# Kernel tuning notes

Hardware: AMD Instinct MI355X
Metric: run time of the kernel (lower is better)

## Reference

```python
import jax, jax.numpy as jnp
from jax import lax
import numpy as np

T, B, I, H, L, O = 512, 64, 256, 512, 2, 256


def _lstm_layer(x_seq, h0, c0, W_ih, W_hh, b_ih, b_hh):
    # x_seq: [T,B,in], W_ih: [4H,in], W_hh: [4H,H]
    pre = jnp.einsum('tbi,gi->tbg', x_seq, W_ih) + b_ih  # [T,B,4H]

    def step(carry, p):
        h, c = carry
        g = p + h @ W_hh.T + b_hh          # [B,4H], PyTorch gate order i,f,g,o
        i, f, gg, o = jnp.split(g, 4, axis=-1)
        i = jax.nn.sigmoid(i)
        f = jax.nn.sigmoid(f)
        gg = jnp.tanh(gg)
        o = jax.nn.sigmoid(o)
        c = f * c + i * gg
        h = o * jnp.tanh(c)
        return (h, c), h

    _, hs = lax.scan(step, (h0, c0), pre)
    return hs  # [T,B,H]


def setup_inputs() -> dict:
    key = jax.random.key(0)
    ks = jax.random.split(key, 12)
    s = 1.0 / np.sqrt(H)
    u = lambda k, shape: jax.random.uniform(k, shape, jnp.float32, -s, s)
    inp = {
        'input': jax.random.normal(ks[0], (T, B, I), jnp.float32),
        'hidden_cell': jnp.zeros((2, L, B, H), jnp.float32),
        'W_ih0': u(ks[1], (4 * H, I)),
        'W_hh0': u(ks[2], (4 * H, H)),
        'b_ih0': u(ks[3], (4 * H,)),
        'b_hh0': u(ks[4], (4 * H,)),
        'W_ih1': u(ks[5], (4 * H, H)),
        'W_hh1': u(ks[6], (4 * H, H)),
        'b_ih1': u(ks[7], (4 * H,)),
        'b_hh1': u(ks[8], (4 * H,)),
        'W_out': u(ks[9], (O, H)),
        'b_out': u(ks[10], (O,)),
    }
    return inp


def reference(input, hidden_cell, W_ih0, W_hh0, b_ih0, b_hh0,
              W_ih1, W_hh1, b_ih1, b_hh1, W_out, b_out):
    h0, c0 = hidden_cell[0], hidden_cell[1]  # each [L,B,H]
    hs0 = _lstm_layer(input, h0[0], c0[0], W_ih0, W_hh0, b_ih0, b_hh0)
    hs1 = _lstm_layer(hs0, h0[1], c0[1], W_ih1, W_hh1, b_ih1, b_hh1)
    # c2o applied to output at final timestep
    return hs1[-1] @ W_out.T + b_out  # [B,O]
```

## Files before the change

kernel.cpp:

```cpp
#include <hip/hip_runtime.h>

typedef _Float16 half8 __attribute__((ext_vector_type(8)));
typedef _Float16 half4 __attribute__((ext_vector_type(4)));
typedef float floatx4 __attribute__((ext_vector_type(4)));
typedef unsigned uintx4 __attribute__((ext_vector_type(4)));
typedef unsigned long long u64;

#define T_STEPS 512
#define IN_DIM 256
#define HID 512
#define RING 8


__device__ inline float sig_f(float x) { return 1.f / (1.f + __expf(-x)); }
__device__ inline float tanh_f(float x) {
  float t = __expf(-2.f * fabsf(x));
  return copysignf((1.f - t) / (1.f + t), x);
}
__device__ inline unsigned umin_(unsigned a, unsigned b) { return a < b ? a : b; }

__device__ inline void cstore_pair(_Float16* p, float a, float b) {
  union { unsigned u; _Float16 h[2]; } pk;
  pk.h[0] = (_Float16)a; pk.h[1] = (_Float16)b;
  __hip_atomic_store((unsigned*)p, pk.u, __ATOMIC_RELAXED, __HIP_MEMORY_SCOPE_AGENT);
}
__device__ inline void cstore64(_Float16* p, u64 v) {
  __hip_atomic_store((u64*)p, v, __ATOMIC_RELAXED, __HIP_MEMORY_SCOPE_AGENT);
}
__device__ inline u64 cload64(const _Float16* p) {
  return __hip_atomic_load((const u64*)p, __ATOMIC_RELAXED, __HIP_MEMORY_SCOPE_AGENT);
}
__device__ inline half8 cload_h8(const _Float16* p) {
  union { u64 u[2]; half8 v; } r;
  r.u[0] = cload64(p);
  r.u[1] = cload64(p + 4);
  return r.v;
}

__device__ inline void ldfrag16(const char* b0, half8 (&r)[16]) {
  const char* b1 = b0 + 4096;
  const char* b2 = b0 + 8192;
  const char* b3 = b0 + 12288;
  floatx4 t0, t1, t2, t3, t4, t5, t6, t7, t8, t9, t10, t11, t12, t13, t14, t15;
  asm volatile(
      "global_load_dwordx4 %0, %16, off sc0 sc1\n\t"
      "global_load_dwordx4 %1, %16, off offset:1024 sc0 sc1\n\t"
      "global_load_dwordx4 %2, %16, off offset:2048 sc0 sc1\n\t"
      "global_load_dwordx4 %3, %16, off offset:3072 sc0 sc1\n\t"
      "global_load_dwordx4 %4, %17, off sc0 sc1\n\t"
      "global_load_dwordx4 %5, %17, off offset:1024 sc0 sc1\n\t"
      "global_load_dwordx4 %6, %17, off offset:2048 sc0 sc1\n\t"
      "global_load_dwordx4 %7, %17, off offset:3072 sc0 sc1\n\t"
      "global_load_dwordx4 %8, %18, off sc0 sc1\n\t"
      "global_load_dwordx4 %9, %18, off offset:1024 sc0 sc1\n\t"
      "global_load_dwordx4 %10, %18, off offset:2048 sc0 sc1\n\t"
      "global_load_dwordx4 %11, %18, off offset:3072 sc0 sc1\n\t"
      "global_load_dwordx4 %12, %19, off sc0 sc1\n\t"
      "global_load_dwordx4 %13, %19, off offset:1024 sc0 sc1\n\t"
      "global_load_dwordx4 %14, %19, off offset:2048 sc0 sc1\n\t"
      "global_load_dwordx4 %15, %19, off offset:3072 sc0 sc1\n\t"
      "s_waitcnt vmcnt(0)"
      : "=&v"(t0), "=&v"(t1), "=&v"(t2), "=&v"(t3),
        "=&v"(t4), "=&v"(t5), "=&v"(t6), "=&v"(t7),
        "=&v"(t8), "=&v"(t9), "=&v"(t10), "=&v"(t11),
        "=&v"(t12), "=&v"(t13), "=&v"(t14), "=&v"(t15)
      : "v"(b0), "v"(b1), "v"(b2), "v"(b3)
      : "memory");
  r[0] = __builtin_bit_cast(half8, t0);   r[1] = __builtin_bit_cast(half8, t1);
  r[2] = __builtin_bit_cast(half8, t2);   r[3] = __builtin_bit_cast(half8, t3);
  r[4] = __builtin_bit_cast(half8, t4);   r[5] = __builtin_bit_cast(half8, t5);
  r[6] = __builtin_bit_cast(half8, t6);   r[7] = __builtin_bit_cast(half8, t7);
  r[8] = __builtin_bit_cast(half8, t8);   r[9] = __builtin_bit_cast(half8, t9);
  r[10] = __builtin_bit_cast(half8, t10); r[11] = __builtin_bit_cast(half8, t11);
  r[12] = __builtin_bit_cast(half8, t12); r[13] = __builtin_bit_cast(half8, t13);
  r[14] = __builtin_bit_cast(half8, t14); r[15] = __builtin_bit_cast(half8, t15);
}

__device__ inline void waitf4(const unsigned* fg, unsigned tg) {
  if (tg == 0) return;
  const unsigned* p = fg + (threadIdx.x & 63) * 32;
  int it = 0;
  for (;;) {
    floatx4 t;
    asm volatile("global_load_dwordx4 %0, %1, off sc0 sc1\n\t"
                 "s_waitcnt vmcnt(0)"
                 : "=&v"(t) : "v"(p) : "memory");
    uintx4 u = __builtin_bit_cast(uintx4, t);
    unsigned m = umin_(umin_(u.x, u.y), umin_(u.z, u.w));
    if (__all((int)(m >= tg))) return;
    if (++it > 4) __builtin_amdgcn_s_sleep(1);
  }
}

__device__ inline bool waitf4_dual(const unsigned* fg1, unsigned tg1,
                                   const unsigned* fg0, unsigned tg0) {
  const unsigned* p1 = fg1 + (threadIdx.x & 63) * 32;
  const unsigned* p0 = fg0 + (threadIdx.x & 63) * 32;
  unsigned m1, m0v;
  int it = 0;
  for (;;) {
    floatx4 t1, t0;
    asm volatile("global_load_dwordx4 %0, %2, off sc0 sc1\n\t"
                 "global_load_dwordx4 %1, %3, off sc0 sc1\n\t"
                 "s_waitcnt vmcnt(0)"
                 : "=&v"(t1), "=&v"(t0)
                 : "v"(p1), "v"(p0)
                 : "memory");
    uintx4 u1 = __builtin_bit_cast(uintx4, t1);
    uintx4 u0 = __builtin_bit_cast(uintx4, t0);
    m1 = umin_(umin_(u1.x, u1.y), umin_(u1.z, u1.w));
    m0v = umin_(umin_(u0.x, u0.y), umin_(u0.z, u0.w));
    if (__all((int)(m1 >= tg1))) break;
    if (++it > 4) __builtin_amdgcn_s_sleep(1);
  }
  return (bool)__all((int)(m0v >= tg0));
}

__device__ inline floatx4 mfma16(half8 a, half8 b, floatx4 c) {
  return __builtin_amdgcn_mfma_f32_16x16x32_f16(a, b, c, 0, 0, 0);
}

__global__ void init_kernel(const float* __restrict__ x, const float* __restrict__ hc,
                            _Float16* __restrict__ x16, _Float16* __restrict__ h0b,
                            _Float16* __restrict__ h1b, unsigned* __restrict__ flagbase) {
  size_t i = (size_t)blockIdx.x * blockDim.x + threadIdx.x;
  size_t stride = (size_t)gridDim.x * blockDim.x;
  const size_t nch = (size_t)T_STEPS * 64 * 32;
  for (size_t n = i; n < nch; n += stride) {
    size_t tr = n >> 5;
    int cc = (int)(n & 31);
    int row = (int)(tr & 63);
    size_t t = tr >> 6;
    const float* src = x + (tr * 256 + (size_t)cc * 8);
    floatx4 v0 = *(const floatx4*)src;
    floatx4 v1 = *(const floatx4*)(src + 4);
    half8 h;
    h[0] = (_Float16)v0.x; h[1] = (_Float16)v0.y; h[2] = (_Float16)v0.z; h[3] = (_Float16)v0.w;
    h[4] = (_Float16)v1.x; h[5] = (_Float16)v1.y; h[6] = (_Float16)v1.z; h[7] = (_Float16)v1.w;
    _Float16* dstp = x16 + t * 16384 + (size_t)(row >> 4) * 4096 +
                     (size_t)(cc >> 2) * 512 + (size_t)((row & 15) + 16 * (cc & 3)) * 8;
    *(half8*)dstp = h;
  }
  if (i < 8192) {
    int which = (int)(i >> 12);
    int idx = (int)(i & 4095);
    int m = idx >> 6, cc = idx & 63;
    const float* src = hc + (size_t)which * 32768 + (size_t)m * 512 + (size_t)cc * 8;
    union { u64 u[2]; half8 v; } pk;
#pragma unroll
    for (int e = 0; e < 8; ++e) pk.v[e] = (_Float16)src[e];
    _Float16* base = which ? (h1b + 32768) : (h0b + (size_t)(RING - 1) * 32768);
    _Float16* dstp = base + (size_t)(m >> 4) * 8192 + (size_t)(cc >> 2) * 512 +
                     (size_t)((m & 15) + 16 * (cc & 3)) * 8;
    cstore64(dstp, pk.u[0]);
    cstore64(dstp + 4, pk.u[1]);
  }
  if (i < 4096) {
    __hip_atomic_store(flagbase + i, 0u, __ATOMIC_RELAXED, __HIP_MEMORY_SCOPE_AGENT);
  }
}

__global__ __launch_bounds__(256, 1) void lstm_kernel(
    const _Float16* __restrict__ x16, _Float16* __restrict__ h0b, _Float16* __restrict__ h1b,
    unsigned* __restrict__ flags0, unsigned* __restrict__ flags1,
    const float* __restrict__ W_ih0, const float* __restrict__ W_hh0,
    const float* __restrict__ b_ih0, const float* __restrict__ b_hh0,
    const float* __restrict__ W_ih1, const float* __restrict__ W_hh1,
    const float* __restrict__ b_ih1, const float* __restrict__ b_hh1,
    const float* __restrict__ W_out, const float* __restrict__ b_out,
    const float* __restrict__ hc, float* __restrict__ out) {
  __shared__ __align__(16) _Float16 wlds[32 * 1032];

  const int bq = blockIdx.x;
  const bool isL0 = bq < 64;
  const int q = isL0 ? bq : bq - 64;
  const int col0 = q * 8;
  const int Ka = isL0 ? IN_DIM : HID;
  const int K = Ka + HID;
  const int WP = K + 8;
  const int layer = isL0 ? 0 : 1;
  const float* Wa = isL0 ? W_ih0 : W_ih1;
  const float* Wb = isL0 ? W_hh0 : W_hh1;
  const float* bia = isL0 ? b_ih0 : b_ih1;
  const float* bib = isL0 ? b_hh0 : b_hh1;

  for (int idx = threadIdx.x; idx < 32 * K; idx += 256) {
    int r = idx / K;
    int k = idx - r * K;
    int g = r >> 3, j = r & 7;
    int grow = g * HID + col0 + j;
    float w = (k < Ka) ? Wa[(size_t)grow * Ka + k] : Wb[(size_t)grow * HID + (k - Ka)];
    wlds[r * WP + k] = (_Float16)w;
  }
  __syncthreads();

  const int lane = threadIdx.x & 63;
  const int wv = threadIdx.x >> 6;
  const int lrow = lane & 15;
  const int kq = (lane >> 4) * 8;
  const int m0 = wv * 16;
  const _Float16* wrow0 = wlds + lrow * WP;
  const _Float16* wrow1 = wlds + (16 + lrow) * WP;

  half8 breg0[16], breg1[16];
#pragma unroll
  for (int c = 0; c < 16; ++c) {
    breg0[c] = *(const half8*)(wrow0 + Ka + c * 32 + kq);
    breg1[c] = *(const half8*)(wrow1 + Ka + c * 32 + kq);
  }

  const int bsel = lrow >> 3;
  const int jc = lrow & 7;
  const int rbase = m0 + ((lane >> 4) << 2) + 2 * bsel;
  const int colg = col0 + jc;
  const float bi_ = bia[colg] + bib[colg];
  const float bf_ = bia[HID + colg] + bib[HID + colg];
  const float bg_ = bia[2 * HID + colg] + bib[2 * HID + colg];
  const float bo_ = bia[3 * HID + colg] + bib[3 * HID + colg];
  float cst0 = hc[(size_t)(2 + layer) * 32768 + (size_t)(rbase + 0) * HID + colg];
  float cst1 = hc[(size_t)(2 + layer) * 32768 + (size_t)(rbase + 1) * HID + colg];

  unsigned* myflag = (isL0 ? flags0 : flags1) + q * 32 + wv;

  const size_t rd_off = (size_t)wv * 16384 + (size_t)lane * 16;
  const size_t st_off = (size_t)wv * 8192 + (size_t)(q >> 2) * 512 +
                        (size_t)((rbase & 15) + ((q & 3) << 4)) * 8 + jc;

  bool skip0 = false;

  for (int t = 0; t < T_STEPS; ++t) {
    floatx4 acc0 = {0.f, 0.f, 0.f, 0.f};
    floatx4 acc1 = {0.f, 0.f, 0.f, 0.f};
    _Float16* dst;
    half8 f[16];

    if (isL0) {
      const _Float16* xw = x16 + (size_t)t * 16384 + (size_t)wv * 4096 + (size_t)lane * 8;
#pragma unroll
      for (int c = 0; c < 8; ++c) {
        half8 a = *(const half8*)(xw + c * 512);
        half8 b0v = *(const half8*)(wrow0 + c * 32 + kq);
        half8 b1v = *(const half8*)(wrow1 + c * 32 + kq);
        acc0 = mfma16(a, b0v, acc0);
        acc1 = mfma16(a, b1v, acc1);
      }
      if (threadIdx.x < 64) waitf4(flags0, (unsigned)t);
      else if (threadIdx.x < 128) waitf4(flags1, (t >= RING) ? (unsigned)(t - RING + 1) : 0u);
      __syncthreads();
      asm volatile("" ::: "memory");
      const char* a1p = (const char*)(h0b + (size_t)((t - 1) & (RING - 1)) * 32768) + rd_off;
      ldfrag16(a1p, f);
#pragma unroll
      for (int c = 0; c < 16; ++c) {
        acc0 = mfma16(f[c], breg0[c], acc0);
        acc1 = mfma16(f[c], breg1[c], acc1);
      }
      dst = h0b + (size_t)(t & (RING - 1)) * 32768;
    } else {
      if (threadIdx.x < 64 && !skip0) waitf4(flags0, (unsigned)(t + 1));
      __syncthreads();
      asm volatile("" ::: "memory");
      const char* a0p = (const char*)(h0b + (size_t)(t & (RING - 1)) * 32768) + rd_off;
      ldfrag16(a0p, f);
#pragma unroll
      for (int c = 0; c < 16; ++c) {
        half8 b0v = *(const half8*)(wrow0 + c * 32 + kq);
        half8 b1v = *(const half8*)(wrow1 + c * 32 + kq);
        acc0 = mfma16(f[c], b0v, acc0);
        acc1 = mfma16(f[c], b1v, acc1);
      }
      if (threadIdx.x < 64)
        skip0 = waitf4_dual(flags1, (unsigned)t, flags0, (unsigned)(t + 2));
      __syncthreads();
      asm volatile("" ::: "memory");
      const char* a1p = (const char*)(h1b + (size_t)((t - 1) & 1) * 32768) + rd_off;
      ldfrag16(a1p, f);
#pragma unroll
      for (int c = 0; c < 16; ++c) {
        acc0 = mfma16(f[c], breg0[c], acc0);
        acc1 = mfma16(f[c], breg1[c], acc1);
      }
      dst = h1b + (size_t)(t & 1) * 32768;
    }

    float s00 = __shfl_xor(bsel ? (float)acc0[0] : (float)acc0[2], 8);
    float s01 = __shfl_xor(bsel ? (float)acc0[1] : (float)acc0[3], 8);
    float s10 = __shfl_xor(bsel ? (float)acc1[0] : (float)acc1[2], 8);
    float s11 = __shfl_xor(bsel ? (float)acc1[1] : (float)acc1[3], 8);
    float hv0, hv1;
    {
      float o0 = bsel ? (float)acc0[2] : (float)acc0[0];
      float o1 = bsel ? (float)acc1[2] : (float)acc1[0];
      float gi = bsel ? s00 : o0;
      float gf = bsel ? o0 : s00;
      float gg = bsel ? s10 : o1;
      float go = bsel ? o1 : s10;
      float c = sig_f(gf + bf_) * cst0 + sig_f(gi + bi_) * tanh_f(gg + bg_);
      cst0 = c;
      hv0 = sig_f(go + bo_) * tanh_f(c);
    }
    {
      float o0 = bsel ? (float)acc0[3] : (float)acc0[1];
      float o1 = bsel ? (float)acc1[3] : (float)acc1[1];
      float gi = bsel ? s01 : o0;
      float gf = bsel ? o0 : s01;
      float gg = bsel ? s11 : o1;
      float go = bsel ? o1 : s11;
      float c = sig_f(gf + bf_) * cst1 + sig_f(gi + bi_) * tanh_f(gg + bg_);
      cst1 = c;
      hv1 = sig_f(go + bo_) * tanh_f(c);
    }
    float hx0 = __shfl_xor(hv0, 1);
    float hx1 = __shfl_xor(hv1, 1);
    if ((jc & 1) == 0) {
      _Float16* sb = dst + st_off;
      cstore_pair(sb, hv0, hx0);
      cstore_pair(sb + 8, hv1, hx1);
    }

    asm volatile("s_waitcnt vmcnt(0)" ::: "memory");
    if ((threadIdx.x & 63) == 0) {
      __hip_atomic_store(myflag, (unsigned)(t + 1), __ATOMIC_RELAXED,
                         __HIP_MEMORY_SCOPE_AGENT);
    }
    asm volatile("" ::: "memory");
  }

  if (isL0) {
    if (threadIdx.x < 64) waitf4(flags1, (unsigned)T_STEPS);
    __syncthreads();
    asm volatile("" ::: "memory");
    const int oc = q * 4 + (threadIdx.x & 3);
    const int m = threadIdx.x >> 2;
    const float* wrow = W_out + (size_t)oc * HID;
    const _Float16* hbase = h1b + 32768;
    float sum = 0.f;
#pragma unroll 4
    for (int hh = 0; hh < 64; ++hh) {
      const _Float16* cp = hbase + (size_t)(m >> 4) * 8192 + (size_t)(hh >> 2) * 512 +
                           (size_t)((m & 15) + 16 * (hh & 3)) * 8;
      half8 hvv = cload_h8(cp);
#pragma unroll
      for (int e = 0; e < 8; ++e) sum += (float)hvv[e] * wrow[hh * 8 + e];
    }
    out[m * 256 + oc] = sum + b_out[oc];
  }
}

extern "C" void kernel_launch(void* const* d_in, const int* in_sizes, int n_in,
                              void* d_out, int out_size, void* d_ws, size_t ws_size,
                              hipStream_t stream) {
  const float* x     = (const float*)d_in[0];
  const float* hc    = (const float*)d_in[1];
  const float* W_ih0 = (const float*)d_in[2];
  const float* W_hh0 = (const float*)d_in[3];
  const float* b_ih0 = (const float*)d_in[4];
  const float* b_hh0 = (const float*)d_in[5];
  const float* W_ih1 = (const float*)d_in[6];
  const float* W_hh1 = (const float*)d_in[7];
  const float* b_ih1 = (const float*)d_in[8];
  const float* b_hh1 = (const float*)d_in[9];
  const float* W_out = (const float*)d_in[10];
  const float* b_out = (const float*)d_in[11];
  float* out = (float*)d_out;

  char* ws = (char*)d_ws;
  _Float16* x16 = (_Float16*)ws;
  _Float16* h0b = (_Float16*)(ws + 16777216);
  _Float16* h1b = (_Float16*)(ws + 16777216 + 8 * 65536);
  unsigned* flags0 = (unsigned*)(ws + 16777216 + 10 * 65536);
  unsigned* flags1 = (unsigned*)(ws + 16777216 + 10 * 65536 + 8192);

  init_kernel<<<2048, 256, 0, stream>>>(x, hc, x16, h0b, h1b, flags0);
  lstm_kernel<<<128, 256, 0, stream>>>(x16, h0b, h1b, flags0, flags1,
                                       W_ih0, W_hh0, b_ih0, b_hh0,
                                       W_ih1, W_hh1, b_ih1, b_hh1,
                                       W_out, b_out, hc, out);
}
```

Measured before the change: 1.818 ms.

## Replace block-wide barriers with per-wave flag polling and early flag publication

Each wave now polls only the single flag of the matching wave in the other blocks, instead of wave 0 polling all flags and then a __syncthreads. The flag loads are issued before the MFMA work so their latency overlaps compute. Layer-1 publishes its step flag as soon as it has read its layer-0 input, rather than after writing h, which loosens the ring-buffer coupling with layer 0. A sentinel flag value marks final completion before the output projection. The risk is subtle ordering races: layer-1 writes h1 after signalling, so the final wait depends on the sentinel value.

```diff
diff --git a/kernel.cpp b/kernel.cpp
--- a/kernel.cpp
+++ b/kernel.cpp
@@ -1,7 +1,6 @@
 #include <hip/hip_runtime.h>
 
 typedef _Float16 half8 __attribute__((ext_vector_type(8)));
-typedef _Float16 half4 __attribute__((ext_vector_type(4)));
 typedef float floatx4 __attribute__((ext_vector_type(4)));
 typedef unsigned uintx4 __attribute__((ext_vector_type(4)));
 typedef unsigned long long u64;
@@ -76,8 +75,20 @@
   r[14] = __builtin_bit_cast(half8, t14); r[15] = __builtin_bit_cast(half8, t15);
 }
 
+__device__ inline void waitpw(const unsigned* p, unsigned tg) {
+  if (tg == 0) return;
+  int it = 0;
+  for (;;) {
+    unsigned v;
+    asm volatile("global_load_dword %0, %1, off sc0 sc1\n\t"
+                 "s_waitcnt vmcnt(0)"
+                 : "=&v"(v) : "v"(p) : "memory");
+    if (__all((int)(v >= tg))) return;
+    if (++it > 4) __builtin_amdgcn_s_sleep(1);
+  }
+}
+
 __device__ inline void waitf4(const unsigned* fg, unsigned tg) {
-  if (tg == 0) return;
   const unsigned* p = fg + (threadIdx.x & 63) * 32;
   int it = 0;
   for (;;) {
@@ -90,30 +101,6 @@
     if (__all((int)(m >= tg))) return;
     if (++it > 4) __builtin_amdgcn_s_sleep(1);
   }
-}
-
-__device__ inline bool waitf4_dual(const unsigned* fg1, unsigned tg1,
-                                   const unsigned* fg0, unsigned tg0) {
-  const unsigned* p1 = fg1 + (threadIdx.x & 63) * 32;
-  const unsigned* p0 = fg0 + (threadIdx.x & 63) * 32;
-  unsigned m1, m0v;
-  int it = 0;
-  for (;;) {
-    floatx4 t1, t0;
-    asm volatile("global_load_dwordx4 %0, %2, off sc0 sc1\n\t"
-                 "global_load_dwordx4 %1, %3, off sc0 sc1\n\t"
-                 "s_waitcnt vmcnt(0)"
-                 : "=&v"(t1), "=&v"(t0)
-                 : "v"(p1), "v"(p0)
-                 : "memory");
-    uintx4 u1 = __builtin_bit_cast(uintx4, t1);
-    uintx4 u0 = __builtin_bit_cast(uintx4, t0);
-    m1 = umin_(umin_(u1.x, u1.y), umin_(u1.z, u1.w));
-    m0v = umin_(umin_(u0.x, u0.y), umin_(u0.z, u0.w));
-    if (__all((int)(m1 >= tg1))) break;
-    if (++it > 4) __builtin_amdgcn_s_sleep(1);
-  }
-  return (bool)__all((int)(m0v >= tg0));
 }
 
 __device__ inline floatx4 mfma16(half8 a, half8 b, floatx4 c) {
@@ -198,7 +185,6 @@
   const int wv = threadIdx.x >> 6;
   const int lrow = lane & 15;
   const int kq = (lane >> 4) * 8;
-  const int m0 = wv * 16;
   const _Float16* wrow0 = wlds + lrow * WP;
   const _Float16* wrow1 = wlds + (16 + lrow) * WP;
 
@@ -211,7 +197,7 @@
 
   const int bsel = lrow >> 3;
   const int jc = lrow & 7;
-  const int rbase = m0 + ((lane >> 4) << 2) + 2 * bsel;
+  const int rbase = wv * 16 + ((lane >> 4) << 2) + 2 * bsel;
   const int colg = col0 + jc;
   const float bi_ = bia[colg] + bib[colg];
   const float bf_ = bia[HID + colg] + bib[HID + colg];
@@ -221,6 +207,8 @@
   float cst1 = hc[(size_t)(2 + layer) * 32768 + (size_t)(rbase + 1) * HID + colg];
 
   unsigned* myflag = (isL0 ? flags0 : flags1) + q * 32 + wv;
+  const unsigned* pw0 = flags0 + lane * 32 + wv;
+  const unsigned* pw1 = flags1 + lane * 32 + wv;
 
   const size_t rd_off = (size_t)wv * 16384 + (size_t)lane * 16;
   const size_t st_off = (size_t)wv * 8192 + (size_t)(q >> 2) * 512 +
@@ -235,6 +223,11 @@
     half8 f[16];
 
     if (isL0) {
+      unsigned s0 = 0xffffffffu, s1 = 0xffffffffu;
+      asm volatile("global_load_dword %0, %2, off sc0 sc1\n\t"
+                   "global_load_dword %1, %3, off sc0 sc1"
+                   : "=&v"(s0), "=&v"(s1)
+                   : "v"(pw0), "v"(pw1) : "memory");
       const _Float16* xw = x16 + (size_t)t * 16384 + (size_t)wv * 4096 + (size_t)lane * 8;
 #pragma unroll
       for (int c = 0; c < 8; ++c) {
@@ -244,10 +237,22 @@
         acc0 = mfma16(a, b0v, acc0);
         acc1 = mfma16(a, b1v, acc1);
       }
-      if (threadIdx.x < 64) waitf4(flags0, (unsigned)t);
-      else if (threadIdx.x < 128) waitf4(flags1, (t >= RING) ? (unsigned)(t - RING + 1) : 0u);
-      __syncthreads();
-      asm volatile("" ::: "memory");
+      asm volatile("s_waitcnt vmcnt(0)" ::: "memory");
+      __builtin_amdgcn_sched_barrier(0);
+      {
+        const unsigned need0 = (unsigned)t;
+        const unsigned need1 = (t >= 8) ? (unsigned)(t - 7) : 0u;
+        int it = 0;
+        while (!__all((int)((s0 >= need0) & (s1 >= need1)))) {
+          if (++it > 4) __builtin_amdgcn_s_sleep(1);
+          asm volatile("global_load_dword %0, %2, off sc0 sc1\n\t"
+                       "global_load_dword %1, %3, off sc0 sc1\n\t"
+                       "s_waitcnt vmcnt(0)"
+                       : "=&v"(s0), "=&v"(s1)
+                       : "v"(pw0), "v"(pw1) : "memory");
+          __builtin_amdgcn_sched_barrier(0);
+        }
+      }
       const char* a1p = (const char*)(h0b + (size_t)((t - 1) & (RING - 1)) * 32768) + rd_off;
       ldfrag16(a1p, f);
 #pragma unroll
@@ -257,11 +262,17 @@
       }
       dst = h0b + (size_t)(t & (RING - 1)) * 32768;
     } else {
-      if (threadIdx.x < 64 && !skip0) waitf4(flags0, (unsigned)(t + 1));
-      __syncthreads();
-      asm volatile("" ::: "memory");
+      if (!skip0) waitpw(pw0, (unsigned)(t + 1));
       const char* a0p = (const char*)(h0b + (size_t)(t & (RING - 1)) * 32768) + rd_off;
       ldfrag16(a0p, f);
+      if (lane == 0)
+        __hip_atomic_store(myflag, (unsigned)(t + 1), __ATOMIC_RELAXED,
+                           __HIP_MEMORY_SCOPE_AGENT);
+      unsigned sp = 0xffffffffu, s0 = 0xffffffffu;
+      asm volatile("global_load_dword %0, %2, off sc0 sc1\n\t"
+                   "global_load_dword %1, %3, off sc0 sc1"
+                   : "=&v"(sp), "=&v"(s0)
+                   : "v"(pw1), "v"(pw0) : "memory");
 #pragma unroll
       for (int c = 0; c < 16; ++c) {
         half8 b0v = *(const half8*)(wrow0 + c * 32 + kq);
@@ -269,10 +280,22 @@
         acc0 = mfma16(f[c], b0v, acc0);
         acc1 = mfma16(f[c], b1v, acc1);
       }
-      if (threadIdx.x < 64)
-        skip0 = waitf4_dual(flags1, (unsigned)t, flags0, (unsigned)(t + 2));
-      __syncthreads();
-      asm volatile("" ::: "memory");
+      asm volatile("s_waitcnt vmcnt(0)" ::: "memory");
+      __builtin_amdgcn_sched_barrier(0);
+      {
+        const unsigned need = (unsigned)(t + 1);
+        int it = 0;
+        while (!__all((int)(sp >= need))) {
+          if (++it > 4) __builtin_amdgcn_s_sleep(1);
+          asm volatile("global_load_dword %0, %2, off sc0 sc1\n\t"
+                       "global_load_dword %1, %3, off sc0 sc1\n\t"
+                       "s_waitcnt vmcnt(0)"
+                       : "=&v"(sp), "=&v"(s0)
+                       : "v"(pw1), "v"(pw0) : "memory");
+          __builtin_amdgcn_sched_barrier(0);
+        }
+        skip0 = (bool)__all((int)(s0 >= (unsigned)(t + 2)));
+      }
       const char* a1p = (const char*)(h1b + (size_t)((t - 1) & 1) * 32768) + rd_off;
       ldfrag16(a1p, f);
 #pragma unroll
@@ -318,16 +341,20 @@
       cstore_pair(sb + 8, hv1, hx1);
     }
 
+    if (isL0) {
+      asm volatile("s_waitcnt vmcnt(0)" ::: "memory");
+      if (lane == 0)
+        __hip_atomic_store(myflag, (unsigned)(t + 1), __ATOMIC_RELAXED,
+                           __HIP_MEMORY_SCOPE_AGENT);
+    }
+  }
+
+  if (!isL0) {
     asm volatile("s_waitcnt vmcnt(0)" ::: "memory");
-    if ((threadIdx.x & 63) == 0) {
-      __hip_atomic_store(myflag, (unsigned)(t + 1), __ATOMIC_RELAXED,
-                         __HIP_MEMORY_SCOPE_AGENT);
-    }
-    asm volatile("" ::: "memory");
-  }
-
-  if (isL0) {
-    if (threadIdx.x < 64) waitf4(flags1, (unsigned)T_STEPS);
+    if (lane == 0)
+      __hip_atomic_store(myflag, 1023u, __ATOMIC_RELAXED, __HIP_MEMORY_SCOPE_AGENT);
+  } else {
+    if (threadIdx.x < 64) waitf4(flags1, 1023u);
     __syncthreads();
     asm volatile("" ::: "memory");
     const int oc = q * 4 + (threadIdx.x & 3);
```

After: 3.126 ms. 72.0% more time.

## Prefetch next-step layer-0 hidden state in layer-1 blocks before flag publish

Applied to the files above, without the earlier changes.

Layer-1 blocks now broadcast the dual-wait result through LDS to all threads. When layer 0 is already known to be two steps ahead, they issue the global loads for the next step's layer-0 h fragment right after storing h. Those loads stay in flight across the flag store, so the next iteration can skip its wait and barrier and just drain vmcnt. The trade is sixteen extra live vector registers of prefetch state and fragile inline-asm vmcnt accounting.

```diff
diff --git a/kernel.cpp b/kernel.cpp
--- a/kernel.cpp
+++ b/kernel.cpp
@@ -1,7 +1,6 @@
 #include <hip/hip_runtime.h>
 
 typedef _Float16 half8 __attribute__((ext_vector_type(8)));
-typedef _Float16 half4 __attribute__((ext_vector_type(4)));
 typedef float floatx4 __attribute__((ext_vector_type(4)));
 typedef unsigned uintx4 __attribute__((ext_vector_type(4)));
 typedef unsigned long long u64;
@@ -37,35 +36,37 @@
   return r.v;
 }
 
+#define LDF16_LOADS                                             \
+  "global_load_dwordx4 %0, %16, off sc0 sc1\n\t"                \
+  "global_load_dwordx4 %1, %16, off offset:1024 sc0 sc1\n\t"    \
+  "global_load_dwordx4 %2, %16, off offset:2048 sc0 sc1\n\t"    \
+  "global_load_dwordx4 %3, %16, off offset:3072 sc0 sc1\n\t"    \
+  "global_load_dwordx4 %4, %17, off sc0 sc1\n\t"                \
+  "global_load_dwordx4 %5, %17, off offset:1024 sc0 sc1\n\t"    \
+  "global_load_dwordx4 %6, %17, off offset:2048 sc0 sc1\n\t"    \
+  "global_load_dwordx4 %7, %17, off offset:3072 sc0 sc1\n\t"    \
+  "global_load_dwordx4 %8, %18, off sc0 sc1\n\t"                \
+  "global_load_dwordx4 %9, %18, off offset:1024 sc0 sc1\n\t"    \
+  "global_load_dwordx4 %10, %18, off offset:2048 sc0 sc1\n\t"   \
+  "global_load_dwordx4 %11, %18, off offset:3072 sc0 sc1\n\t"   \
+  "global_load_dwordx4 %12, %19, off sc0 sc1\n\t"               \
+  "global_load_dwordx4 %13, %19, off offset:1024 sc0 sc1\n\t"   \
+  "global_load_dwordx4 %14, %19, off offset:2048 sc0 sc1\n\t"   \
+  "global_load_dwordx4 %15, %19, off offset:3072 sc0 sc1"
+
 __device__ inline void ldfrag16(const char* b0, half8 (&r)[16]) {
   const char* b1 = b0 + 4096;
   const char* b2 = b0 + 8192;
   const char* b3 = b0 + 12288;
   floatx4 t0, t1, t2, t3, t4, t5, t6, t7, t8, t9, t10, t11, t12, t13, t14, t15;
-  asm volatile(
-      "global_load_dwordx4 %0, %16, off sc0 sc1\n\t"
-      "global_load_dwordx4 %1, %16, off offset:1024 sc0 sc1\n\t"
-      "global_load_dwordx4 %2, %16, off offset:2048 sc0 sc1\n\t"
-      "global_load_dwordx4 %3, %16, off offset:3072 sc0 sc1\n\t"
-      "global_load_dwordx4 %4, %17, off sc0 sc1\n\t"
-      "global_load_dwordx4 %5, %17, off offset:1024 sc0 sc1\n\t"
-      "global_load_dwordx4 %6, %17, off offset:2048 sc0 sc1\n\t"
-      "global_load_dwordx4 %7, %17, off offset:3072 sc0 sc1\n\t"
-      "global_load_dwordx4 %8, %18, off sc0 sc1\n\t"
-      "global_load_dwordx4 %9, %18, off offset:1024 sc0 sc1\n\t"
-      "global_load_dwordx4 %10, %18, off offset:2048 sc0 sc1\n\t"
-      "global_load_dwordx4 %11, %18, off offset:3072 sc0 sc1\n\t"
-      "global_load_dwordx4 %12, %19, off sc0 sc1\n\t"
-      "global_load_dwordx4 %13, %19, off offset:1024 sc0 sc1\n\t"
-      "global_load_dwordx4 %14, %19, off offset:2048 sc0 sc1\n\t"
-      "global_load_dwordx4 %15, %19, off offset:3072 sc0 sc1\n\t"
-      "s_waitcnt vmcnt(0)"
-      : "=&v"(t0), "=&v"(t1), "=&v"(t2), "=&v"(t3),
-        "=&v"(t4), "=&v"(t5), "=&v"(t6), "=&v"(t7),
-        "=&v"(t8), "=&v"(t9), "=&v"(t10), "=&v"(t11),
-        "=&v"(t12), "=&v"(t13), "=&v"(t14), "=&v"(t15)
-      : "v"(b0), "v"(b1), "v"(b2), "v"(b3)
-      : "memory");
+  asm volatile(LDF16_LOADS "\n\t"
+               "s_waitcnt vmcnt(0)"
+               : "=&v"(t0), "=&v"(t1), "=&v"(t2), "=&v"(t3),
+                 "=&v"(t4), "=&v"(t5), "=&v"(t6), "=&v"(t7),
+                 "=&v"(t8), "=&v"(t9), "=&v"(t10), "=&v"(t11),
+                 "=&v"(t12), "=&v"(t13), "=&v"(t14), "=&v"(t15)
+               : "v"(b0), "v"(b1), "v"(b2), "v"(b3)
+               : "memory");
   r[0] = __builtin_bit_cast(half8, t0);   r[1] = __builtin_bit_cast(half8, t1);
   r[2] = __builtin_bit_cast(half8, t2);   r[3] = __builtin_bit_cast(half8, t3);
   r[4] = __builtin_bit_cast(half8, t4);   r[5] = __builtin_bit_cast(half8, t5);
@@ -170,6 +171,7 @@
     const float* __restrict__ W_out, const float* __restrict__ b_out,
     const float* __restrict__ hc, float* __restrict__ out) {
   __shared__ __align__(16) _Float16 wlds[32 * 1032];
+  __shared__ unsigned skLDS[2];
 
   const int bq = blockIdx.x;
   const bool isL0 = bq < 64;
@@ -198,7 +200,6 @@
   const int wv = threadIdx.x >> 6;
   const int lrow = lane & 15;
   const int kq = (lane >> 4) * 8;
-  const int m0 = wv * 16;
   const _Float16* wrow0 = wlds + lrow * WP;
   const _Float16* wrow1 = wlds + (16 + lrow) * WP;
 
@@ -211,7 +212,7 @@
 
   const int bsel = lrow >> 3;
   const int jc = lrow & 7;
-  const int rbase = m0 + ((lane >> 4) << 2) + 2 * bsel;
+  const int rbase = wv * 16 + ((lane >> 4) << 2) + 2 * bsel;
   const int colg = col0 + jc;
   const float bi_ = bia[colg] + bib[colg];
   const float bf_ = bia[HID + colg] + bib[HID + colg];
@@ -226,13 +227,17 @@
   const size_t st_off = (size_t)wv * 8192 + (size_t)(q >> 2) * 512 +
                         (size_t)((rbase & 15) + ((q & 3) << 4)) * 8 + jc;
 
-  bool skip0 = false;
+  bool skip0r = false;
+  bool pref = false;
+  half8 f[16];
+  floatx4 pf0, pf1, pf2, pf3, pf4, pf5, pf6, pf7,
+          pf8, pf9, pf10, pf11, pf12, pf13, pf14, pf15;
 
   for (int t = 0; t < T_STEPS; ++t) {
     floatx4 acc0 = {0.f, 0.f, 0.f, 0.f};
     floatx4 acc1 = {0.f, 0.f, 0.f, 0.f};
     _Float16* dst;
-    half8 f[16];
+    unsigned skv = 0;
 
     if (isL0) {
       const _Float16* xw = x16 + (size_t)t * 16384 + (size_t)wv * 4096 + (size_t)lane * 8;
@@ -257,11 +262,29 @@
       }
       dst = h0b + (size_t)(t & (RING - 1)) * 32768;
     } else {
-      if (threadIdx.x < 64 && !skip0) waitf4(flags0, (unsigned)(t + 1));
-      __syncthreads();
-      asm volatile("" ::: "memory");
-      const char* a0p = (const char*)(h0b + (size_t)(t & (RING - 1)) * 32768) + rd_off;
-      ldfrag16(a0p, f);
+      if (!pref) {
+        if (threadIdx.x < 64 && !skip0r) waitf4(flags0, (unsigned)(t + 1));
+        __syncthreads();
+        asm volatile("" ::: "memory");
+        const char* a0p = (const char*)(h0b + (size_t)(t & (RING - 1)) * 32768) + rd_off;
+        ldfrag16(a0p, f);
+      } else {
+        asm volatile("s_waitcnt vmcnt(0)"
+                     : "+v"(pf0), "+v"(pf1), "+v"(pf2), "+v"(pf3),
+                       "+v"(pf4), "+v"(pf5), "+v"(pf6), "+v"(pf7),
+                       "+v"(pf8), "+v"(pf9), "+v"(pf10), "+v"(pf11),
+                       "+v"(pf12), "+v"(pf13), "+v"(pf14), "+v"(pf15)
+                     :: "memory");
+        __builtin_amdgcn_sched_barrier(0);
+        f[0] = __builtin_bit_cast(half8, pf0);   f[1] = __builtin_bit_cast(half8, pf1);
+        f[2] = __builtin_bit_cast(half8, pf2);   f[3] = __builtin_bit_cast(half8, pf3);
+        f[4] = __builtin_bit_cast(half8, pf4);   f[5] = __builtin_bit_cast(half8, pf5);
+        f[6] = __builtin_bit_cast(half8, pf6);   f[7] = __builtin_bit_cast(half8, pf7);
+        f[8] = __builtin_bit_cast(half8, pf8);   f[9] = __builtin_bit_cast(half8, pf9);
+        f[10] = __builtin_bit_cast(half8, pf10); f[11] = __builtin_bit_cast(half8, pf11);
+        f[12] = __builtin_bit_cast(half8, pf12); f[13] = __builtin_bit_cast(half8, pf13);
+        f[14] = __builtin_bit_cast(half8, pf14); f[15] = __builtin_bit_cast(half8, pf15);
+      }
 #pragma unroll
       for (int c = 0; c < 16; ++c) {
         half8 b0v = *(const half8*)(wrow0 + c * 32 + kq);
@@ -269,10 +292,13 @@
         acc0 = mfma16(f[c], b0v, acc0);
         acc1 = mfma16(f[c], b1v, acc1);
       }
-      if (threadIdx.x < 64)
-        skip0 = waitf4_dual(flags1, (unsigned)t, flags0, (unsigned)(t + 2));
+      if (threadIdx.x < 64) {
+        bool sk = waitf4_dual(flags1, (unsigned)t, flags0, (unsigned)(t + 2));
+        if (threadIdx.x == 0) skLDS[t & 1] = sk ? 1u : 0u;
+      }
       __syncthreads();
       asm volatile("" ::: "memory");
+      skv = skLDS[t & 1];
       const char* a1p = (const char*)(h1b + (size_t)((t - 1) & 1) * 32768) + rd_off;
       ldfrag16(a1p, f);
 #pragma unroll
@@ -318,12 +344,40 @@
       cstore_pair(sb + 8, hv1, hx1);
     }
 
-    asm volatile("s_waitcnt vmcnt(0)" ::: "memory");
-    if ((threadIdx.x & 63) == 0) {
-      __hip_atomic_store(myflag, (unsigned)(t + 1), __ATOMIC_RELAXED,
-                         __HIP_MEMORY_SCOPE_AGENT);
-    }
-    asm volatile("" ::: "memory");
+    if (isL0) {
+      asm volatile("s_waitcnt vmcnt(0)" ::: "memory");
+      if ((threadIdx.x & 63) == 0) {
+        __hip_atomic_store(myflag, (unsigned)(t + 1), __ATOMIC_RELAXED,
+                           __HIP_MEMORY_SCOPE_AGENT);
+      }
+      asm volatile("" ::: "memory");
+    } else {
+      __builtin_amdgcn_sched_barrier(0);
+      if (skv && t < T_STEPS - 1) {
+        const char* nb0 = (const char*)(h0b + (size_t)((t + 1) & (RING - 1)) * 32768) + rd_off;
+        const char* nb1 = nb0 + 4096;
+        const char* nb2 = nb0 + 8192;
+        const char* nb3 = nb0 + 12288;
+        asm volatile(LDF16_LOADS "\n\t"
+                     "s_waitcnt vmcnt(16)"
+                     : "=&v"(pf0), "=&v"(pf1), "=&v"(pf2), "=&v"(pf3),
+                       "=&v"(pf4), "=&v"(pf5), "=&v"(pf6), "=&v"(pf7),
+                       "=&v"(pf8), "=&v"(pf9), "=&v"(pf10), "=&v"(pf11),
+                       "=&v"(pf12), "=&v"(pf13), "=&v"(pf14), "=&v"(pf15)
+                     : "v"(nb0), "v"(nb1), "v"(nb2), "v"(nb3)
+                     : "memory");
+        pref = true;
+      } else {
+        asm volatile("s_waitcnt vmcnt(0)" ::: "memory");
+        pref = false;
+      }
+      skip0r = (skv != 0);
+      if ((threadIdx.x & 63) == 0) {
+        __hip_atomic_store(myflag, (unsigned)(t + 1), __ATOMIC_RELAXED,
+                           __HIP_MEMORY_SCOPE_AGENT);
+      }
+      asm volatile("" ::: "memory");
+    }
   }
 
   if (isL0) {
```

Result: slower. 2.391 ms (+31.5%).
